# Kernel optimization log

Measured on AMD Instinct MI355X. Metric: run time of the kernel, lower is better.

## Reference

```python
import jax, jax.numpy as jnp
import numpy as np

B, LQ, LKV = 4, 512, 8192
Q_DIM, KV_DIM = 1024, 512
QK_CH, V_CH, N_HEADS = 256, 256, 8
EPS = 1e-5


def _layernorm(x, g, b):
    m = jnp.mean(x, axis=-1, keepdims=True)
    v = jnp.mean(jnp.square(x - m), axis=-1, keepdims=True)
    return (x - m) * jax.lax.rsqrt(v + EPS) * g + b


def setup_inputs() -> dict:
    key = jax.random.key(0)
    ks = jax.random.split(key, 8)
    hidden_states = jax.random.normal(ks[0], (B, LQ, Q_DIM), dtype=jnp.float32)
    inputs = jax.random.normal(ks[1], (B, LKV, KV_DIM), dtype=jnp.float32)
    # Linear weights stored as [in, out] for x @ W
    Wq = jax.random.normal(ks[2], (Q_DIM, QK_CH), dtype=jnp.float32) * (1.0 / np.sqrt(Q_DIM))
    Wk = jax.random.normal(ks[3], (KV_DIM, QK_CH), dtype=jnp.float32) * (1.0 / np.sqrt(KV_DIM))
    Wv = jax.random.normal(ks[4], (KV_DIM, V_CH), dtype=jnp.float32) * (1.0 / np.sqrt(KV_DIM))
    bq = jnp.zeros((QK_CH,), jnp.float32)
    bk = jax.random.normal(ks[5], (QK_CH,), dtype=jnp.float32) * 0.02
    bv = jax.random.normal(ks[6], (V_CH,), dtype=jnp.float32) * 0.02
    ln1_g = jnp.ones((Q_DIM,), jnp.float32)
    ln1_b = jnp.zeros((Q_DIM,), jnp.float32)
    ln2_g = jnp.ones((KV_DIM,), jnp.float32)
    ln2_b = jnp.zeros((KV_DIM,), jnp.float32)
    return dict(hidden_states=hidden_states, inputs=inputs,
                ln1_g=ln1_g, ln1_b=ln1_b, ln2_g=ln2_g, ln2_b=ln2_b,
                Wq=Wq, bq=bq, Wk=Wk, bk=bk, Wv=Wv, bv=bv)


def reference(hidden_states, inputs, ln1_g, ln1_b, ln2_g, ln2_b,
              Wq, bq, Wk, bk, Wv, bv):
    H = N_HEADS
    dqk = QK_CH // H
    dv = V_CH // H
    hs = _layernorm(hidden_states, ln1_g, ln1_b)          # [B,LQ,Q_DIM]
    inp = _layernorm(inputs, ln2_g, ln2_b)                # [B,LKV,KV_DIM]
    q = (hs @ Wq + bq).reshape(B, LQ, H, dqk)             # [B,LQ,H,dqk]
    k = (inp @ Wk + bk).reshape(B, LKV, H, dqk)           # [B,LKV,H,dqk]
    v = (inp @ Wv + bv).reshape(B, LKV, H, dv)            # [B,LKV,H,dv]
    scores = jnp.einsum('bqhd,bkhd->bhqk', q, k) / np.sqrt(dqk).astype(np.float32)
    probs = jax.nn.softmax(scores, axis=-1)               # [B,H,LQ,LKV] (materialized, as in torch)
    ctx = jnp.einsum('bhqk,bkhd->bqhd', probs, v)         # [B,LQ,H,dv]
    return ctx.reshape(B, LQ, H * dv)
```

## Files before the change

### kernel.cpp

```cpp
#include <hip/hip_runtime.h>
#include <hip/hip_bf16.h>
#include <math.h>

#define NB    4
#define LQ    512
#define LKV   8192
#define QDIM  1024
#define KVDIM 512
#define NH    8
#define EPS_LN 1e-5f

typedef __attribute__((ext_vector_type(8))) short bf16x8;
typedef __attribute__((ext_vector_type(4))) float f32x4;

static __device__ __forceinline__ ushort f2bf(float x) {
    unsigned int u = __builtin_bit_cast(unsigned int, x);
    u += 0x7FFFu + ((u >> 16) & 1u);
    return (ushort)(u >> 16);
}
static __device__ __forceinline__ float bf2f(ushort b) {
    return __builtin_bit_cast(float, (unsigned int)b << 16);
}
static __device__ __forceinline__ void gld_lds16(const ushort* g, ushort* l) {
    __builtin_amdgcn_global_load_lds(
        (const __attribute__((address_space(1))) unsigned int*)g,
        (__attribute__((address_space(3))) unsigned int*)l, 16, 0, 0);
}

template<int K>
__global__ __launch_bounds__(256) void ln_norm_kernel(
    const float* __restrict__ x, const float* __restrict__ g,
    const float* __restrict__ bta, ushort* __restrict__ y)
{
    const int lane = threadIdx.x & 63;
    const int row  = blockIdx.x * 4 + (threadIdx.x >> 6);
    const float* xp = x + (size_t)row * K;
    constexpr int NV = K / 256;
    float4 v[NV];
    float s = 0.f;
#pragma unroll
    for (int i = 0; i < NV; ++i) {
        v[i] = *(const float4*)(xp + lane * 4 + i * 256);
        s += v[i].x + v[i].y + v[i].z + v[i].w;
    }
#pragma unroll
    for (int o = 1; o < 64; o <<= 1) s += __shfl_xor(s, o, 64);
    const float mu = s * (1.0f / K);
    float vs = 0.f;
#pragma unroll
    for (int i = 0; i < NV; ++i) {
        float dx = v[i].x - mu, dy = v[i].y - mu, dz = v[i].z - mu, dw = v[i].w - mu;
        vs += dx * dx + dy * dy + dz * dz + dw * dw;
    }
#pragma unroll
    for (int o = 1; o < 64; o <<= 1) vs += __shfl_xor(vs, o, 64);
    const float rs = rsqrtf(vs * (1.0f / K) + EPS_LN);
#pragma unroll
    for (int i = 0; i < NV; ++i) {
        const float4 gv = *(const float4*)(g   + lane * 4 + i * 256);
        const float4 bv = *(const float4*)(bta + lane * 4 + i * 256);
        ushort4 o;
        o.x = f2bf((v[i].x - mu) * rs * gv.x + bv.x);
        o.y = f2bf((v[i].y - mu) * rs * gv.y + bv.y);
        o.z = f2bf((v[i].z - mu) * rs * gv.z + bv.z);
        o.w = f2bf((v[i].w - mu) * rs * gv.w + bv.w);
        *(ushort4*)(y + (size_t)row * K + lane * 4 + i * 256) = o;
    }
}

__global__ __launch_bounds__(256) void wt_convert_kernel(
    const float* __restrict__ Wq, const float* __restrict__ Wk,
    const float* __restrict__ Wv, ushort* __restrict__ WtQ,
    ushort* __restrict__ WtKV)
{
    const int n = blockIdx.x;
    const int t = threadIdx.x;
    if (n < 512) {
        const float* src; int col;
        if (n < 256) { src = Wk; col = n; } else { src = Wv; col = n - 256; }
#pragma unroll
        for (int i = 0; i < 2; ++i) {
            const int k = t + i * 256;
            WtKV[(size_t)n * 512 + k] = f2bf(src[(size_t)k * 256 + col]);
        }
    } else {
        const int nq = n - 512;
#pragma unroll
        for (int i = 0; i < 4; ++i) {
            const int k = t + i * 256;
            WtQ[(size_t)nq * 1024 + k] = f2bf(Wq[(size_t)k * 256 + nq]);
        }
    }
}

template<int TK, int LOGTOK>
__global__ __launch_bounds__(256) void mfma_gemm_kernel(
    const ushort* __restrict__ A, const ushort* __restrict__ Wt,
    const float* __restrict__ b0, const float* __restrict__ b1,
    ushort* __restrict__ out0, ushort* __restrict__ out1, float oscale)
{
    __shared__ __align__(16) ushort As[128 * 32];
    __shared__ __align__(16) ushort Bs[128 * 32];

    const int t    = threadIdx.x;
    const int lane = t & 63;
    const int w    = t >> 6;
    const int lq   = lane & 15;
    const int lg   = lane >> 4;
    const int wm   = w >> 1;
    const int wn   = w & 1;
    const int bm   = blockIdx.x * 128;
    const int bn   = blockIdx.y * 128;

    const ushort* gA = A  + (size_t)(bm + (t >> 2)) * TK + (t & 3) * 8;
    const ushort* gB = Wt + (size_t)(bn + (t >> 2)) * TK + (t & 3) * 8;
    ushort* lA = As + t * 8;
    ushort* lB = Bs + t * 8;

    f32x4 acc[4][4] = {};

    for (int k0 = 0; k0 < TK; k0 += 32) {
        gld_lds16(gA + k0,                      lA);
        gld_lds16(gA + (size_t)64 * TK + k0,    lA + 2048);
        gld_lds16(gB + k0,                      lB);
        gld_lds16(gB + (size_t)64 * TK + k0,    lB + 2048);
        __syncthreads();

        bf16x8 af[4], bf[4];
#pragma unroll
        for (int mt = 0; mt < 4; ++mt)
            af[mt] = *(const bf16x8*)(As + (wm * 64 + mt * 16 + lq) * 32 + lg * 8);
#pragma unroll
        for (int nt = 0; nt < 4; ++nt)
            bf[nt] = *(const bf16x8*)(Bs + (wn * 64 + nt * 16 + lq) * 32 + lg * 8);
#pragma unroll
        for (int mt = 0; mt < 4; ++mt)
#pragma unroll
            for (int nt = 0; nt < 4; ++nt)
                acc[mt][nt] = __builtin_amdgcn_mfma_f32_16x16x32_bf16(af[mt], bf[nt], acc[mt][nt], 0, 0, 0);
        __syncthreads();
    }

    constexpr int tokmask = (1 << LOGTOK) - 1;
#pragma unroll
    for (int nt = 0; nt < 4; ++nt) {
        const int n = bn + wn * 64 + nt * 16 + lq;
        if (n < 256) {
            const int h = n >> 5, d = n & 31;
            const float bias = b0[n];
#pragma unroll
            for (int mt = 0; mt < 4; ++mt) {
                const int m0   = bm + wm * 64 + mt * 16 + lg * 4;
                const int bidx = m0 >> LOGTOK;
                const int tok  = m0 & tokmask;
                const size_t base = (((size_t)(bidx * NH + h) << LOGTOK) + tok) * 32 + d;
#pragma unroll
                for (int r = 0; r < 4; ++r)
                    out0[base + (size_t)r * 32] = f2bf((acc[mt][nt][r] + bias) * oscale);
            }
        } else {
            const int nv = n - 256;
            const int h = nv >> 5, d = nv & 31;
            const float bias = b1[nv];
#pragma unroll
            for (int mt = 0; mt < 4; ++mt) {
                const int m0   = bm + wm * 64 + mt * 16 + lg * 4;
                const int bidx = m0 >> LOGTOK;
                const int tok  = m0 & tokmask;
                ushort4 o;
                o.x = f2bf(acc[mt][nt][0] + bias);
                o.y = f2bf(acc[mt][nt][1] + bias);
                o.z = f2bf(acc[mt][nt][2] + bias);
                o.w = f2bf(acc[mt][nt][3] + bias);
                *(ushort4*)(out1 + ((size_t)(bidx * NH + h) * 32 + d) * LKV + tok) = o;
            }
        }
    }
}

__global__ __launch_bounds__(512, 1) void attn_mfma_kernel(
    const ushort* __restrict__ Qb,
    const ushort* __restrict__ Kb,
    const ushort* __restrict__ Vt,
    float* __restrict__ Out)
{
    const int bh = blockIdx.y, b = bh >> 3, h = bh & 7;
    const int qt = blockIdx.x;
    const int t  = threadIdx.x, w = t >> 6, lane = t & 63;
    const int lq = lane & 15, lg = lane >> 4;

    __shared__ __align__(16) ushort Pb[8][64][40];
    __shared__ float mbuf[8][64], lbuf[8][64], glbuf[64];

    bf16x8 qfrag[4];
    const size_t qbase = ((size_t)bh * LQ + qt * 64) * 32;
#pragma unroll
    for (int n = 0; n < 4; ++n)
        qfrag[n] = *(const bf16x8*)(Qb + qbase + (size_t)(n * 16 + lq) * 32 + lg * 8);

    const ushort* KpA = Kb + ((size_t)bh * LKV + w * 1024 + lq) * 32 + lg * 8;
    const ushort* VpA = Vt + ((size_t)bh * 32 + lq) * LKV + w * 1024 + lg * 8;

    f32x4 oacc[2][4] = {};
    float m_run[4] = {-1e30f, -1e30f, -1e30f, -1e30f};
    float l_run[4] = {0.f, 0.f, 0.f, 0.f};
    ushort* myP = &Pb[w][0][0];

    bf16x8 kf0 = *(const bf16x8*)(KpA);
    bf16x8 kf1 = *(const bf16x8*)(KpA + 16 * 32);
    bf16x8 vf0 = *(const bf16x8*)(VpA);
    bf16x8 vf1 = *(const bf16x8*)(VpA + (size_t)16 * LKV);

    for (int kt = 0; kt < 1024; kt += 32) {
        const bf16x8 kc0 = kf0, kc1 = kf1, vc0 = vf0, vc1 = vf1;
        const int nk = (kt + 32 < 1024) ? kt + 32 : 0;
        kf0 = *(const bf16x8*)(KpA + (size_t)nk * 32);
        kf1 = *(const bf16x8*)(KpA + (size_t)(nk + 16) * 32);
        vf0 = *(const bf16x8*)(VpA + nk);
        vf1 = *(const bf16x8*)(VpA + (size_t)16 * LKV + nk);

        const f32x4 zero = {0.f, 0.f, 0.f, 0.f};
        f32x4 s[2][4];
#pragma unroll
        for (int n = 0; n < 4; ++n) {
            s[0][n] = __builtin_amdgcn_mfma_f32_16x16x32_bf16(kc0, qfrag[n], zero, 0, 0, 0);
            s[1][n] = __builtin_amdgcn_mfma_f32_16x16x32_bf16(kc1, qfrag[n], zero, 0, 0, 0);
        }

        uint2 pw[2][4];
#pragma unroll
        for (int n = 0; n < 4; ++n) {
            float pm = s[0][n][0];
            pm = fmaxf(pm, s[0][n][1]); pm = fmaxf(pm, s[0][n][2]); pm = fmaxf(pm, s[0][n][3]);
            pm = fmaxf(pm, s[1][n][0]); pm = fmaxf(pm, s[1][n][1]);
            pm = fmaxf(pm, s[1][n][2]); pm = fmaxf(pm, s[1][n][3]);
            pm = fmaxf(pm, __shfl_xor(pm, 16));
            pm = fmaxf(pm, __shfl_xor(pm, 32));
            const float mnew = fmaxf(m_run[n], pm);
            const float a = __expf(m_run[n] - mnew);
            m_run[n] = mnew;

            float ps = 0.f;
#pragma unroll
            for (int m = 0; m < 2; ++m) {
                ushort pb[4];
#pragma unroll
                for (int r = 0; r < 4; ++r) {
                    const float p = __expf(s[m][n][r] - mnew);
                    pb[r] = f2bf(p);
                    ps += bf2f(pb[r]);
                }
                pw[m][n].x = (unsigned int)pb[0] | ((unsigned int)pb[1] << 16);
                pw[m][n].y = (unsigned int)pb[2] | ((unsigned int)pb[3] << 16);
            }
            ps += __shfl_xor(ps, 16);
            ps += __shfl_xor(ps, 32);
            l_run[n] = l_run[n] * a + ps;
            oacc[0][n] *= a;
            oacc[1][n] *= a;
        }

#pragma unroll
        for (int n = 0; n < 4; ++n)
#pragma unroll
            for (int m = 0; m < 2; ++m)
                *(uint2*)(myP + (n * 16 + lq) * 40 + m * 16 + lg * 4) = pw[m][n];

        bf16x8 pf[4];
#pragma unroll
        for (int n = 0; n < 4; ++n)
            pf[n] = *(const bf16x8*)(myP + (size_t)(n * 16 + lq) * 40 + lg * 8);

#pragma unroll
        for (int n = 0; n < 4; ++n) {
            oacc[0][n] = __builtin_amdgcn_mfma_f32_16x16x32_bf16(vc0, pf[n], oacc[0][n], 0, 0, 0);
            oacc[1][n] = __builtin_amdgcn_mfma_f32_16x16x32_bf16(vc1, pf[n], oacc[1][n], 0, 0, 0);
        }
    }

    if (lg == 0) {
#pragma unroll
        for (int n = 0; n < 4; ++n) {
            mbuf[w][n * 16 + lq] = m_run[n];
            lbuf[w][n * 16 + lq] = l_run[n];
        }
    }
    __syncthreads();

    float* Ob = (float*)&Pb[0][0][0];
#pragma unroll
    for (int n = 0; n < 4; ++n) {
        const int q = n * 16 + lq;
        float gm = mbuf[0][q];
#pragma unroll
        for (int j = 1; j < 8; ++j) gm = fmaxf(gm, mbuf[j][q]);
        float gl = 0.f;
#pragma unroll
        for (int j = 0; j < 8; ++j) gl += lbuf[j][q] * __expf(mbuf[j][q] - gm);
        const float f = __expf(m_run[n] - gm);
        oacc[0][n] *= f;
        oacc[1][n] *= f;
        if (w == 0 && lg == 0) glbuf[q] = gl;
    }

    if (w >= 4) {
        const int wj = w - 4;
#pragma unroll
        for (int n = 0; n < 4; ++n)
#pragma unroll
            for (int m = 0; m < 2; ++m)
                *(f32x4*)&Ob[((size_t)wj * 64 + n * 16 + lq) * 40 + m * 16 + lg * 4] = oacc[m][n];
    }
    __syncthreads();
    if (w < 4) {
#pragma unroll
        for (int n = 0; n < 4; ++n)
#pragma unroll
            for (int m = 0; m < 2; ++m) {
                float* p = &Ob[((size_t)w * 64 + n * 16 + lq) * 40 + m * 16 + lg * 4];
                f32x4 v = *(f32x4*)p;
                v += oacc[m][n];
                *(f32x4*)p = v;
            }
    }
    __syncthreads();
    {
        const int q = t >> 3, d0 = (t & 7) * 4;
        f32x4 sum = *(const f32x4*)&Ob[((size_t)0 * 64 + q) * 40 + d0];
        sum += *(const f32x4*)&Ob[((size_t)1 * 64 + q) * 40 + d0];
        sum += *(const f32x4*)&Ob[((size_t)2 * 64 + q) * 40 + d0];
        sum += *(const f32x4*)&Ob[((size_t)3 * 64 + q) * 40 + d0];
        sum *= (1.0f / glbuf[q]);
        *(f32x4*)(Out + ((size_t)b * LQ + qt * 64 + q) * 256 + h * 32 + d0) = sum;
    }
}

extern "C" void kernel_launch(void* const* d_in, const int* in_sizes, int n_in,
                              void* d_out, int out_size, void* d_ws, size_t ws_size,
                              hipStream_t stream)
{
    const float* hidden = (const float*)d_in[0];
    const float* inputs = (const float*)d_in[1];
    const float* ln1g   = (const float*)d_in[2];
    const float* ln1b   = (const float*)d_in[3];
    const float* ln2g   = (const float*)d_in[4];
    const float* ln2b   = (const float*)d_in[5];
    const float* Wq     = (const float*)d_in[6];
    const float* bq     = (const float*)d_in[7];
    const float* Wk     = (const float*)d_in[8];
    const float* bk     = (const float*)d_in[9];
    const float* Wv     = (const float*)d_in[10];
    const float* bv     = (const float*)d_in[11];
    float* out = (float*)d_out;

    char* wsb = (char*)d_ws;
    ushort* qb   = (ushort*)(wsb);
    ushort* WtKV = (ushort*)(wsb + (1u << 20));
    ushort* WtQ  = (ushort*)(wsb + (1u << 20) + (512u << 10));
    ushort* kb   = (ushort*)(wsb + (2u << 20));
    ushort* vt   = (ushort*)(wsb + (18u << 20));
    ushort* Abf  = (ushort*)(wsb + (34u << 20));
    ushort* AbfQ = Abf;

    const float qscale = 0.17677669529663687f;

    ln_norm_kernel<QDIM><<<NB * LQ / 4, 256, 0, stream>>>(hidden, ln1g, ln1b, AbfQ);
    wt_convert_kernel<<<768, 256, 0, stream>>>(Wq, Wk, Wv, WtQ, WtKV);
    {
        dim3 g(NB * LQ / 128, 256 / 128);
        mfma_gemm_kernel<QDIM, 9><<<g, 256, 0, stream>>>(AbfQ, WtQ, bq, nullptr,
                                                         qb, nullptr, qscale);
    }
    ln_norm_kernel<KVDIM><<<NB * LKV / 4, 256, 0, stream>>>(inputs, ln2g, ln2b, Abf);
    {
        dim3 g(NB * LKV / 128, 512 / 128);
        mfma_gemm_kernel<KVDIM, 13><<<g, 256, 0, stream>>>(Abf, WtKV, bk, bv,
                                                           kb, vt, 1.0f);
    }
    {
        dim3 g(LQ / 64, NB * NH);
        attn_mfma_kernel<<<g, 512, 0, stream>>>(qb, kb, vt, out);
    }
}
```

Measured before the change: 246.7 us.

## Retile attention to 32 queries per block, swizzle GEMM LDS, use exp2 and packed bf16

Measured after the change: 223.6 us. -9.3%, faster.

```diff
diff --git a/kernel.cpp b/kernel.cpp
--- a/kernel.cpp
+++ b/kernel.cpp
@@ -18,9 +18,24 @@
     u += 0x7FFFu + ((u >> 16) & 1u);
     return (ushort)(u >> 16);
 }
-static __device__ __forceinline__ float bf2f(ushort b) {
-    return __builtin_bit_cast(float, (unsigned int)b << 16);
-}
+
+#if __has_builtin(__builtin_amdgcn_cvt_pk_bf16_f32)
+static __device__ __forceinline__ unsigned int pk_bf16(float a, float b) {
+    auto r = __builtin_amdgcn_cvt_pk_bf16_f32(a, b);
+    return __builtin_bit_cast(unsigned int, r);
+}
+#else
+static __device__ __forceinline__ unsigned int pk_bf16(float a, float b) {
+    return (unsigned int)f2bf(a) | ((unsigned int)f2bf(b) << 16);
+}
+#endif
+
+#if __has_builtin(__builtin_amdgcn_exp2f)
+#define EXP2F(x) __builtin_amdgcn_exp2f(x)
+#else
+#define EXP2F(x) exp2f(x)
+#endif
+
 static __device__ __forceinline__ void gld_lds16(const ushort* g, ushort* l) {
     __builtin_amdgcn_global_load_lds(
         (const __attribute__((address_space(1))) unsigned int*)g,
@@ -59,48 +74,46 @@
     for (int i = 0; i < NV; ++i) {
         const float4 gv = *(const float4*)(g   + lane * 4 + i * 256);
         const float4 bv = *(const float4*)(bta + lane * 4 + i * 256);
-        ushort4 o;
-        o.x = f2bf((v[i].x - mu) * rs * gv.x + bv.x);
-        o.y = f2bf((v[i].y - mu) * rs * gv.y + bv.y);
-        o.z = f2bf((v[i].z - mu) * rs * gv.z + bv.z);
-        o.w = f2bf((v[i].w - mu) * rs * gv.w + bv.w);
-        *(ushort4*)(y + (size_t)row * K + lane * 4 + i * 256) = o;
-    }
-}
-
-__global__ __launch_bounds__(256) void wt_convert_kernel(
-    const float* __restrict__ Wq, const float* __restrict__ Wk,
-    const float* __restrict__ Wv, ushort* __restrict__ WtQ,
-    ushort* __restrict__ WtKV)
-{
-    const int n = blockIdx.x;
-    const int t = threadIdx.x;
-    if (n < 512) {
-        const float* src; int col;
-        if (n < 256) { src = Wk; col = n; } else { src = Wv; col = n - 256; }
-#pragma unroll
-        for (int i = 0; i < 2; ++i) {
-            const int k = t + i * 256;
-            WtKV[(size_t)n * 512 + k] = f2bf(src[(size_t)k * 256 + col]);
-        }
-    } else {
-        const int nq = n - 512;
-#pragma unroll
-        for (int i = 0; i < 4; ++i) {
-            const int k = t + i * 256;
-            WtQ[(size_t)nq * 1024 + k] = f2bf(Wq[(size_t)k * 256 + nq]);
-        }
-    }
-}
-
-template<int TK, int LOGTOK>
-__global__ __launch_bounds__(256) void mfma_gemm_kernel(
+        ushort2 o0, o1;
+        unsigned int u0 = pk_bf16((v[i].x - mu) * rs * gv.x + bv.x,
+                                  (v[i].y - mu) * rs * gv.y + bv.y);
+        unsigned int u1 = pk_bf16((v[i].z - mu) * rs * gv.z + bv.z,
+                                  (v[i].w - mu) * rs * gv.w + bv.w);
+        uint2 o; o.x = u0; o.y = u1;
+        *(uint2*)(y + (size_t)row * K + lane * 4 + i * 256) = o;
+    }
+}
+
+__global__ __launch_bounds__(256) void wt_transpose_kernel(
+    const float* __restrict__ src, ushort* __restrict__ dst, int K, int N)
+{
+    __shared__ ushort Ts[64][72];
+    const int t  = threadIdx.x;
+    const int k0 = blockIdx.x * 64;
+    const int n0 = blockIdx.y * 64;
+    const int nl = t & 63;
+#pragma unroll
+    for (int p = 0; p < 16; ++p) {
+        const int kl = p * 4 + (t >> 6);
+        Ts[nl][kl] = f2bf(src[(size_t)(k0 + kl) * N + n0 + nl]);
+    }
+    __syncthreads();
+    const int ck = (t & 7) * 8;
+#pragma unroll
+    for (int p = 0; p < 2; ++p) {
+        const int rn = p * 32 + (t >> 3);
+        *(bf16x8*)(dst + (size_t)(n0 + rn) * K + k0 + ck) = *(const bf16x8*)&Ts[rn][ck];
+    }
+}
+
+__global__ __launch_bounds__(256) void gemm_kv_kernel(
     const ushort* __restrict__ A, const ushort* __restrict__ Wt,
     const float* __restrict__ b0, const float* __restrict__ b1,
-    ushort* __restrict__ out0, ushort* __restrict__ out1, float oscale)
-{
-    __shared__ __align__(16) ushort As[128 * 32];
-    __shared__ __align__(16) ushort Bs[128 * 32];
+    ushort* __restrict__ out0, ushort* __restrict__ out1)
+{
+    __shared__ __align__(16) ushort SM[4][64][72];
+    ushort* As = &SM[0][0][0];
+    ushort* Bs = As + 4096;
 
     const int t    = threadIdx.x;
     const int lane = t & 63;
@@ -112,27 +125,33 @@
     const int bm   = blockIdx.x * 128;
     const int bn   = blockIdx.y * 128;
 
-    const ushort* gA = A  + (size_t)(bm + (t >> 2)) * TK + (t & 3) * 8;
-    const ushort* gB = Wt + (size_t)(bn + (t >> 2)) * TK + (t & 3) * 8;
+    const int srow = t >> 2;
+    const int scol = ((t & 3) ^ ((t >> 3) & 3)) * 8;
+    const ushort* gA = A  + (size_t)(bm + srow) * KVDIM + scol;
+    const ushort* gB = Wt + (size_t)(bn + srow) * KVDIM + scol;
     ushort* lA = As + t * 8;
     ushort* lB = Bs + t * 8;
 
     f32x4 acc[4][4] = {};
 
-    for (int k0 = 0; k0 < TK; k0 += 32) {
-        gld_lds16(gA + k0,                      lA);
-        gld_lds16(gA + (size_t)64 * TK + k0,    lA + 2048);
-        gld_lds16(gB + k0,                      lB);
-        gld_lds16(gB + (size_t)64 * TK + k0,    lB + 2048);
+    for (int k0 = 0; k0 < KVDIM; k0 += 32) {
+        gld_lds16(gA + k0,                       lA);
+        gld_lds16(gA + (size_t)64 * KVDIM + k0,  lA + 2048);
+        gld_lds16(gB + k0,                       lB);
+        gld_lds16(gB + (size_t)64 * KVDIM + k0,  lB + 2048);
         __syncthreads();
 
         bf16x8 af[4], bf[4];
 #pragma unroll
-        for (int mt = 0; mt < 4; ++mt)
-            af[mt] = *(const bf16x8*)(As + (wm * 64 + mt * 16 + lq) * 32 + lg * 8);
-#pragma unroll
-        for (int nt = 0; nt < 4; ++nt)
-            bf[nt] = *(const bf16x8*)(Bs + (wn * 64 + nt * 16 + lq) * 32 + lg * 8);
+        for (int mt = 0; mt < 4; ++mt) {
+            const int m = wm * 64 + mt * 16 + lq;
+            af[mt] = *(const bf16x8*)(As + m * 32 + ((lg ^ ((m >> 1) & 3)) << 3));
+        }
+#pragma unroll
+        for (int nt = 0; nt < 4; ++nt) {
+            const int n = wn * 64 + nt * 16 + lq;
+            bf[nt] = *(const bf16x8*)(Bs + n * 32 + ((lg ^ ((n >> 1) & 3)) << 3));
+        }
 #pragma unroll
         for (int mt = 0; mt < 4; ++mt)
 #pragma unroll
@@ -141,69 +160,155 @@
         __syncthreads();
     }
 
-    constexpr int tokmask = (1 << LOGTOK) - 1;
-#pragma unroll
-    for (int nt = 0; nt < 4; ++nt) {
-        const int n = bn + wn * 64 + nt * 16 + lq;
-        if (n < 256) {
+    if (bn < 256) {
+#pragma unroll
+        for (int nt = 0; nt < 4; ++nt) {
+            const int n = bn + wn * 64 + nt * 16 + lq;
             const int h = n >> 5, d = n & 31;
             const float bias = b0[n];
 #pragma unroll
             for (int mt = 0; mt < 4; ++mt) {
                 const int m0   = bm + wm * 64 + mt * 16 + lg * 4;
-                const int bidx = m0 >> LOGTOK;
-                const int tok  = m0 & tokmask;
-                const size_t base = (((size_t)(bidx * NH + h) << LOGTOK) + tok) * 32 + d;
+                const int bidx = m0 >> 13;
+                const int tok  = m0 & 8191;
+                const size_t base = (((size_t)(bidx * NH + h) << 13) + tok) * 32 + d;
 #pragma unroll
                 for (int r = 0; r < 4; ++r)
-                    out0[base + (size_t)r * 32] = f2bf((acc[mt][nt][r] + bias) * oscale);
-            }
-        } else {
-            const int nv = n - 256;
+                    out0[base + (size_t)r * 32] = f2bf(acc[mt][nt][r] + bias);
+            }
+        }
+    } else {
+        ushort (*Cs)[72] = (ushort(*)[72])&SM[w][0][0];
+#pragma unroll
+        for (int nt = 0; nt < 4; ++nt) {
+            const int n_l = nt * 16 + lq;
+            const float bias = b1[(bn - 256) + wn * 64 + n_l];
+#pragma unroll
+            for (int mt = 0; mt < 4; ++mt) {
+                uint2 o;
+                o.x = pk_bf16(acc[mt][nt][0] + bias, acc[mt][nt][1] + bias);
+                o.y = pk_bf16(acc[mt][nt][2] + bias, acc[mt][nt][3] + bias);
+                *(uint2*)&Cs[n_l][mt * 16 + lg * 4] = o;
+            }
+        }
+        const int r0 = lane >> 3;
+        const int cm = (lane & 7) * 8;
+        const int m0base = bm + wm * 64;
+        const int bidx   = m0base >> 13;
+        const int tokb   = (m0base & 8191) + cm;
+#pragma unroll
+        for (int p = 0; p < 8; ++p) {
+            const int row = p * 8 + r0;
+            const int nv  = (bn - 256) + wn * 64 + row;
             const int h = nv >> 5, d = nv & 31;
-            const float bias = b1[nv];
-#pragma unroll
-            for (int mt = 0; mt < 4; ++mt) {
-                const int m0   = bm + wm * 64 + mt * 16 + lg * 4;
-                const int bidx = m0 >> LOGTOK;
-                const int tok  = m0 & tokmask;
-                ushort4 o;
-                o.x = f2bf(acc[mt][nt][0] + bias);
-                o.y = f2bf(acc[mt][nt][1] + bias);
-                o.z = f2bf(acc[mt][nt][2] + bias);
-                o.w = f2bf(acc[mt][nt][3] + bias);
-                *(ushort4*)(out1 + ((size_t)(bidx * NH + h) * 32 + d) * LKV + tok) = o;
-            }
-        }
-    }
-}
-
-__global__ __launch_bounds__(512, 1) void attn_mfma_kernel(
+            *(bf16x8*)(out1 + ((size_t)(bidx * NH + h) * 32 + d) * LKV + tokb) =
+                *(const bf16x8*)&Cs[row][cm];
+        }
+    }
+}
+
+__global__ __launch_bounds__(256) void gemm_q_kernel(
+    const ushort* __restrict__ A, const ushort* __restrict__ Wt,
+    const float* __restrict__ b0, ushort* __restrict__ out0, float oscale)
+{
+    __shared__ __align__(16) ushort As[64 * 64];
+    __shared__ __align__(16) ushort Bs[64 * 64];
+
+    const int t    = threadIdx.x;
+    const int lane = t & 63;
+    const int w    = t >> 6;
+    const int lq   = lane & 15;
+    const int lg   = lane >> 4;
+    const int wm   = w >> 1;
+    const int wn   = w & 1;
+    const int bm   = blockIdx.x * 64;
+    const int bn   = blockIdx.y * 64;
+
+    const int srow = t >> 3;
+    const int scol = ((t & 7) ^ ((t >> 3) & 7)) * 8;
+    const ushort* gA = A  + (size_t)(bm + srow) * QDIM + scol;
+    const ushort* gB = Wt + (size_t)(bn + srow) * QDIM + scol;
+    ushort* lA = As + t * 8;
+    ushort* lB = Bs + t * 8;
+
+    f32x4 acc[2][2] = {};
+
+    for (int k0 = 0; k0 < QDIM; k0 += 64) {
+        gld_lds16(gA + k0,                      lA);
+        gld_lds16(gA + (size_t)32 * QDIM + k0,  lA + 2048);
+        gld_lds16(gB + k0,                      lB);
+        gld_lds16(gB + (size_t)32 * QDIM + k0,  lB + 2048);
+        __syncthreads();
+#pragma unroll
+        for (int kh = 0; kh < 2; ++kh) {
+            bf16x8 af[2], bf[2];
+#pragma unroll
+            for (int mt = 0; mt < 2; ++mt) {
+                const int m = wm * 32 + mt * 16 + lq;
+                af[mt] = *(const bf16x8*)(As + m * 64 + (((lg + 4 * kh) ^ (m & 7)) << 3));
+            }
+#pragma unroll
+            for (int nt = 0; nt < 2; ++nt) {
+                const int n = wn * 32 + nt * 16 + lq;
+                bf[nt] = *(const bf16x8*)(Bs + n * 64 + (((lg + 4 * kh) ^ (n & 7)) << 3));
+            }
+#pragma unroll
+            for (int mt = 0; mt < 2; ++mt)
+#pragma unroll
+                for (int nt = 0; nt < 2; ++nt)
+                    acc[mt][nt] = __builtin_amdgcn_mfma_f32_16x16x32_bf16(af[mt], bf[nt], acc[mt][nt], 0, 0, 0);
+        }
+        __syncthreads();
+    }
+
+#pragma unroll
+    for (int nt = 0; nt < 2; ++nt) {
+        const int n = bn + wn * 32 + nt * 16 + lq;
+        const int h = n >> 5, d = n & 31;
+        const float bias = b0[n];
+#pragma unroll
+        for (int mt = 0; mt < 2; ++mt) {
+            const int m0   = bm + wm * 32 + mt * 16 + lg * 4;
+            const int bidx = m0 >> 9;
+            const int tok  = m0 & 511;
+            const size_t base = (((size_t)(bidx * NH + h) << 9) + tok) * 32 + d;
+#pragma unroll
+            for (int r = 0; r < 4; ++r)
+                out0[base + (size_t)r * 32] = f2bf((acc[mt][nt][r] + bias) * oscale);
+        }
+    }
+}
+
+__global__ __launch_bounds__(512, 4) void attn_mfma_kernel(
     const ushort* __restrict__ Qb,
     const ushort* __restrict__ Kb,
     const ushort* __restrict__ Vt,
     float* __restrict__ Out)
 {
-    const int bh = blockIdx.y, b = bh >> 3, h = bh & 7;
-    const int qt = blockIdx.x;
-    const int t  = threadIdx.x, w = t >> 6, lane = t & 63;
+    const int bid = blockIdx.x;
+    const int xcd = bid & 7;
+    const int rr  = bid >> 3;
+    const int bh  = ((rr & 3) << 3) | xcd;
+    const int qt  = rr >> 2;
+    const int b = bh >> 3, h = bh & 7;
+    const int t = threadIdx.x, w = t >> 6, lane = t & 63;
     const int lq = lane & 15, lg = lane >> 4;
 
-    __shared__ __align__(16) ushort Pb[8][64][40];
-    __shared__ float mbuf[8][64], lbuf[8][64], glbuf[64];
-
-    bf16x8 qfrag[4];
-    const size_t qbase = ((size_t)bh * LQ + qt * 64) * 32;
-#pragma unroll
-    for (int n = 0; n < 4; ++n)
+    __shared__ __align__(16) ushort Pb[8][32][40];
+    __shared__ float mbuf[8][32], lbuf[8][32], glbuf[32];
+
+    bf16x8 qfrag[2];
+    const size_t qbase = ((size_t)bh * LQ + qt * 32) * 32;
+#pragma unroll
+    for (int n = 0; n < 2; ++n)
         qfrag[n] = *(const bf16x8*)(Qb + qbase + (size_t)(n * 16 + lq) * 32 + lg * 8);
 
     const ushort* KpA = Kb + ((size_t)bh * LKV + w * 1024 + lq) * 32 + lg * 8;
     const ushort* VpA = Vt + ((size_t)bh * 32 + lq) * LKV + w * 1024 + lg * 8;
 
-    f32x4 oacc[2][4] = {};
-    float m_run[4] = {-1e30f, -1e30f, -1e30f, -1e30f};
-    float l_run[4] = {0.f, 0.f, 0.f, 0.f};
+    f32x4 oacc[2][2] = {};
+    float m_run[2] = {-1e30f, -1e30f};
+    float l_run[2] = {0.f, 0.f};
     ushort* myP = &Pb[w][0][0];
 
     bf16x8 kf0 = *(const bf16x8*)(KpA);
@@ -220,38 +325,34 @@
         vf1 = *(const bf16x8*)(VpA + (size_t)16 * LKV + nk);
 
         const f32x4 zero = {0.f, 0.f, 0.f, 0.f};
-        f32x4 s[2][4];
-#pragma unroll
-        for (int n = 0; n < 4; ++n) {
+        f32x4 s[2][2];
+#pragma unroll
+        for (int n = 0; n < 2; ++n) {
             s[0][n] = __builtin_amdgcn_mfma_f32_16x16x32_bf16(kc0, qfrag[n], zero, 0, 0, 0);
             s[1][n] = __builtin_amdgcn_mfma_f32_16x16x32_bf16(kc1, qfrag[n], zero, 0, 0, 0);
         }
 
-        uint2 pw[2][4];
-#pragma unroll
-        for (int n = 0; n < 4; ++n) {
-            float pm = s[0][n][0];
-            pm = fmaxf(pm, s[0][n][1]); pm = fmaxf(pm, s[0][n][2]); pm = fmaxf(pm, s[0][n][3]);
-            pm = fmaxf(pm, s[1][n][0]); pm = fmaxf(pm, s[1][n][1]);
-            pm = fmaxf(pm, s[1][n][2]); pm = fmaxf(pm, s[1][n][3]);
+        uint2 pw[2][2];
+#pragma unroll
+        for (int n = 0; n < 2; ++n) {
+            float pm = fmaxf(fmaxf(fmaxf(s[0][n][0], s[0][n][1]), fmaxf(s[0][n][2], s[0][n][3])),
+                             fmaxf(fmaxf(s[1][n][0], s[1][n][1]), fmaxf(s[1][n][2], s[1][n][3])));
             pm = fmaxf(pm, __shfl_xor(pm, 16));
             pm = fmaxf(pm, __shfl_xor(pm, 32));
             const float mnew = fmaxf(m_run[n], pm);
-            const float a = __expf(m_run[n] - mnew);
+            const float a = EXP2F(m_run[n] - mnew);
             m_run[n] = mnew;
 
             float ps = 0.f;
 #pragma unroll
             for (int m = 0; m < 2; ++m) {
-                ushort pb[4];
-#pragma unroll
-                for (int r = 0; r < 4; ++r) {
-                    const float p = __expf(s[m][n][r] - mnew);
-                    pb[r] = f2bf(p);
-                    ps += bf2f(pb[r]);
-                }
-                pw[m][n].x = (unsigned int)pb[0] | ((unsigned int)pb[1] << 16);
-                pw[m][n].y = (unsigned int)pb[2] | ((unsigned int)pb[3] << 16);
+                float p0 = EXP2F(s[m][n][0] - mnew);
+                float p1 = EXP2F(s[m][n][1] - mnew);
+                float p2 = EXP2F(s[m][n][2] - mnew);
+                float p3 = EXP2F(s[m][n][3] - mnew);
+                ps += (p0 + p1) + (p2 + p3);
+                pw[m][n].x = pk_bf16(p0, p1);
+                pw[m][n].y = pk_bf16(p2, p3);
             }
             ps += __shfl_xor(ps, 16);
             ps += __shfl_xor(ps, 32);
@@ -261,18 +362,18 @@
         }
 
 #pragma unroll
-        for (int n = 0; n < 4; ++n)
+        for (int n = 0; n < 2; ++n)
 #pragma unroll
             for (int m = 0; m < 2; ++m)
                 *(uint2*)(myP + (n * 16 + lq) * 40 + m * 16 + lg * 4) = pw[m][n];
 
-        bf16x8 pf[4];
-#pragma unroll
-        for (int n = 0; n < 4; ++n)
+        bf16x8 pf[2];
+#pragma unroll
+        for (int n = 0; n < 2; ++n)
             pf[n] = *(const bf16x8*)(myP + (size_t)(n * 16 + lq) * 40 + lg * 8);
 
 #pragma unroll
-        for (int n = 0; n < 4; ++n) {
+        for (int n = 0; n < 2; ++n) {
             oacc[0][n] = __builtin_amdgcn_mfma_f32_16x16x32_bf16(vc0, pf[n], oacc[0][n], 0, 0, 0);
             oacc[1][n] = __builtin_amdgcn_mfma_f32_16x16x32_bf16(vc1, pf[n], oacc[1][n], 0, 0, 0);
         }
@@ -280,7 +381,7 @@
 
     if (lg == 0) {
 #pragma unroll
-        for (int n = 0; n < 4; ++n) {
+        for (int n = 0; n < 2; ++n) {
             mbuf[w][n * 16 + lq] = m_run[n];
             lbuf[w][n * 16 + lq] = l_run[n];
         }
@@ -289,15 +390,15 @@
 
     float* Ob = (float*)&Pb[0][0][0];
 #pragma unroll
-    for (int n = 0; n < 4; ++n) {
+    for (int n = 0; n < 2; ++n) {
         const int q = n * 16 + lq;
         float gm = mbuf[0][q];
 #pragma unroll
         for (int j = 1; j < 8; ++j) gm = fmaxf(gm, mbuf[j][q]);
         float gl = 0.f;
 #pragma unroll
-        for (int j = 0; j < 8; ++j) gl += lbuf[j][q] * __expf(mbuf[j][q] - gm);
-        const float f = __expf(m_run[n] - gm);
+        for (int j = 0; j < 8; ++j) gl += lbuf[j][q] * EXP2F(mbuf[j][q] - gm);
+        const float f = EXP2F(m_run[n] - gm);
         oacc[0][n] *= f;
         oacc[1][n] *= f;
         if (w == 0 && lg == 0) glbuf[q] = gl;
@@ -306,18 +407,18 @@
     if (w >= 4) {
         const int wj = w - 4;
 #pragma unroll
-        for (int n = 0; n < 4; ++n)
+        for (int n = 0; n < 2; ++n)
 #pragma unroll
             for (int m = 0; m < 2; ++m)
-                *(f32x4*)&Ob[((size_t)wj * 64 + n * 16 + lq) * 40 + m * 16 + lg * 4] = oacc[m][n];
+                *(f32x4*)&Ob[((size_t)wj * 32 + n * 16 + lq) * 40 + m * 16 + lg * 4] = oacc[m][n];
     }
     __syncthreads();
     if (w < 4) {
 #pragma unroll
-        for (int n = 0; n < 4; ++n)
+        for (int n = 0; n < 2; ++n)
 #pragma unroll
             for (int m = 0; m < 2; ++m) {
-                float* p = &Ob[((size_t)w * 64 + n * 16 + lq) * 40 + m * 16 + lg * 4];
+                float* p = &Ob[((size_t)w * 32 + n * 16 + lq) * 40 + m * 16 + lg * 4];
                 f32x4 v = *(f32x4*)p;
                 v += oacc[m][n];
                 *(f32x4*)p = v;
@@ -325,13 +426,16 @@
     }
     __syncthreads();
     {
-        const int q = t >> 3, d0 = (t & 7) * 4;
-        f32x4 sum = *(const f32x4*)&Ob[((size_t)0 * 64 + q) * 40 + d0];
-        sum += *(const f32x4*)&Ob[((size_t)1 * 64 + q) * 40 + d0];
-        sum += *(const f32x4*)&Ob[((size_t)2 * 64 + q) * 40 + d0];
-        sum += *(const f32x4*)&Ob[((size_t)3 * 64 + q) * 40 + d0];
-        sum *= (1.0f / glbuf[q]);
-        *(f32x4*)(Out + ((size_t)b * LQ + qt * 64 + q) * 256 + h * 32 + d0) = sum;
+        const int q = t >> 4, d0 = (t & 15) * 2;
+        float s0 = 0.f, s1 = 0.f;
+#pragma unroll
+        for (int j = 0; j < 4; ++j) {
+            s0 += Ob[((size_t)j * 32 + q) * 40 + d0];
+            s1 += Ob[((size_t)j * 32 + q) * 40 + d0 + 1];
+        }
+        const float inv = 1.0f / glbuf[q];
+        float2 o; o.x = s0 * inv; o.y = s1 * inv;
+        *(float2*)(Out + ((size_t)b * LQ + qt * 32 + q) * 256 + h * 32 + d0) = o;
     }
 }
 
@@ -362,23 +466,20 @@
     ushort* Abf  = (ushort*)(wsb + (34u << 20));
     ushort* AbfQ = Abf;
 
-    const float qscale = 0.17677669529663687f;
+    const float oscale = 0.2550540226496112f;
 
     ln_norm_kernel<QDIM><<<NB * LQ / 4, 256, 0, stream>>>(hidden, ln1g, ln1b, AbfQ);
-    wt_convert_kernel<<<768, 256, 0, stream>>>(Wq, Wk, Wv, WtQ, WtKV);
+    wt_transpose_kernel<<<dim3(QDIM / 64, 256 / 64), 256, 0, stream>>>(Wq, WtQ, QDIM, 256);
     {
-        dim3 g(NB * LQ / 128, 256 / 128);
-        mfma_gemm_kernel<QDIM, 9><<<g, 256, 0, stream>>>(AbfQ, WtQ, bq, nullptr,
-                                                         qb, nullptr, qscale);
-    }
+        dim3 g(NB * LQ / 64, 256 / 64);
+        gemm_q_kernel<<<g, 256, 0, stream>>>(AbfQ, WtQ, bq, qb, oscale);
+    }
+    wt_transpose_kernel<<<dim3(KVDIM / 64, 256 / 64), 256, 0, stream>>>(Wk, WtKV, KVDIM, 256);
+    wt_transpose_kernel<<<dim3(KVDIM / 64, 256 / 64), 256, 0, stream>>>(Wv, WtKV + (size_t)256 * KVDIM, KVDIM, 256);
     ln_norm_kernel<KVDIM><<<NB * LKV / 4, 256, 0, stream>>>(inputs, ln2g, ln2b, Abf);
     {
         dim3 g(NB * LKV / 128, 512 / 128);
-        mfma_gemm_kernel<KVDIM, 13><<<g, 256, 0, stream>>>(Abf, WtKV, bk, bv,
-                                                           kb, vt, 1.0f);
-    }
-    {
-        dim3 g(LQ / 64, NB * NH);
-        attn_mfma_kernel<<<g, 512, 0, stream>>>(qb, kb, vt, out);
-    }
-}
+        gemm_kv_kernel<<<g, 256, 0, stream>>>(Abf, WtKV, bk, bv, kb, vt);
+    }
+    attn_mfma_kernel<<<512, 512, 0, stream>>>(qb, kb, vt, out);
+}
```
